# Kernel optimization log

Hardware: AMD Instinct MI355X
Metric: run time of the kernel (lower is better)

The kernel has to match this reference:

```python
import jax, jax.numpy as jnp
import numpy as np

R = 16
ALPHA = 32.0


def setup_inputs() -> dict:
    key = jax.random.key(0)
    k1, k2, k3, k4, k5 = jax.random.split(key, 5)
    in_f, out_f = 4096, 11008
    x = jax.random.normal(k1, (8192, in_f), dtype=jnp.float32)
    W = jax.random.normal(k2, (out_f, in_f), dtype=jnp.float32) * 0.02
    bias = jax.random.normal(k3, (out_f,), dtype=jnp.float32) * 0.02
    B = jax.random.normal(k4, (out_f, R), dtype=jnp.float32) * 0.01
    A = jax.random.normal(k5, (R, in_f), dtype=jnp.float32) * 0.01
    return {"x": x, "W": W, "bias": bias, "B": B, "A": A}


def reference(x, W, bias, B, A):
    # Faithful to original: materialize full-rank delta lora_mat = B @ A (out x in),
    # then h = x @ W^T + bias + (x @ lora_mat^T) * (alpha / r).
    lora_mat = jnp.matmul(B, A)                    # [out, in]
    out = jnp.matmul(x, W.T) + bias                # [tokens, out]
    lora_out = jnp.matmul(x, lora_mat.T) * (ALPHA / R)
    return out + lora_out
```

## Files before the change

### kernel.cpp

```cpp
#include <hip/hip_runtime.h>
#include <stdint.h>
#include <stddef.h>

#define M_TOK 8192
#define K_IN  4096
#define N_OUT 11008

typedef __attribute__((ext_vector_type(8))) short   short8;
typedef __attribute__((ext_vector_type(4))) float   floatx4;

#define AS1(p) ((const __attribute__((address_space(1))) void*)(p))
#define AS3(p) ((__attribute__((address_space(3))) void*)(p))

__device__ __forceinline__ unsigned short f2bf_rne(float f) {
  union { float f; unsigned u; } v; v.f = f;
  unsigned r = v.u + 0x7FFFu + ((v.u >> 16) & 1u);
  return (unsigned short)(r >> 16);
}

__device__ __forceinline__ unsigned long long pack4(float a, float b, float c, float d) {
  return (unsigned long long)f2bf_rne(a)
       | ((unsigned long long)f2bf_rne(b) << 16)
       | ((unsigned long long)f2bf_rne(c) << 32)
       | ((unsigned long long)f2bf_rne(d) << 48);
}

__global__ void cast_x_kernel(const float* __restrict__ x,
                              unsigned long long* __restrict__ xb) {
  size_t idx = (size_t)blockIdx.x * blockDim.x + threadIdx.x;
  const float4 v = ((const float4*)x)[idx];
  xb[idx] = pack4(v.x, v.y, v.z, v.w);
}

__global__ void wprime_kernel(const float* __restrict__ W,
                              const float* __restrict__ B,
                              const float* __restrict__ A,
                              unsigned long long* __restrict__ wp) {
  const int o   = blockIdx.x;
  const int col = blockIdx.y * 1024 + threadIdx.x * 4;
  float4 acc = *(const float4*)(W + (size_t)o * K_IN + col);
#pragma unroll
  for (int r = 0; r < 16; ++r) {
    const float b2 = 2.0f * B[o * 16 + r];
    const float4 a4 = *(const float4*)(A + (size_t)r * K_IN + col);
    acc.x += b2 * a4.x; acc.y += b2 * a4.y;
    acc.z += b2 * a4.z; acc.w += b2 * a4.w;
  }
  wp[((size_t)o * K_IN + col) >> 2] = pack4(acc.x, acc.y, acc.z, acc.w);
}

__global__ __launch_bounds__(256) void lora_gemm(
    const unsigned short* __restrict__ Xb,
    const unsigned short* __restrict__ Wp,
    const float* __restrict__ bias,
    float* __restrict__ out) {
  __shared__ __align__(16) unsigned short As[128 * 32];
  __shared__ __align__(16) unsigned short Bs[128 * 32];

  const int tid  = threadIdx.x;
  const int m0   = blockIdx.y * 128;
  const int n0   = blockIdx.x * 128;
  const int wid  = tid >> 6;
  const int lane = tid & 63;
  const int wm   = (wid >> 1) * 64;
  const int wn   = (wid & 1) * 64;
  const int lrow = lane & 15;
  const int quad = lane >> 4;

  floatx4 acc[4][4];
#pragma unroll
  for (int i = 0; i < 4; ++i)
#pragma unroll
    for (int j = 0; j < 4; ++j)
      acc[i][j] = (floatx4){0.f, 0.f, 0.f, 0.f};

  const int r0 = tid >> 2;
  const int s0 = (tid & 3) * 8;
  const unsigned short* pa = Xb + (size_t)(m0 + r0) * K_IN + s0;
  const unsigned short* pb = Wp + (size_t)(n0 + r0) * K_IN + s0;

  const unsigned short* pAf = As + (wm + lrow) * 32 + quad * 8;
  const unsigned short* pBf = Bs + (wn + lrow) * 32 + quad * 8;

  for (int kt = 0; kt < K_IN / 32; ++kt) {
    __builtin_amdgcn_global_load_lds(AS1(pa),                    AS3(As + tid * 8),        16, 0, 0);
    __builtin_amdgcn_global_load_lds(AS1(pa + (size_t)64 * K_IN), AS3(As + tid * 8 + 2048), 16, 0, 0);
    __builtin_amdgcn_global_load_lds(AS1(pb),                    AS3(Bs + tid * 8),        16, 0, 0);
    __builtin_amdgcn_global_load_lds(AS1(pb + (size_t)64 * K_IN), AS3(Bs + tid * 8 + 2048), 16, 0, 0);
    pa += 32; pb += 32;
    __syncthreads();

    short8 a[4], b[4];
#pragma unroll
    for (int mi = 0; mi < 4; ++mi)
      a[mi] = *(const short8*)(pAf + mi * 16 * 32);
#pragma unroll
    for (int ni = 0; ni < 4; ++ni)
      b[ni] = *(const short8*)(pBf + ni * 16 * 32);

#pragma unroll
    for (int mi = 0; mi < 4; ++mi)
#pragma unroll
      for (int ni = 0; ni < 4; ++ni)
        acc[mi][ni] = __builtin_amdgcn_mfma_f32_16x16x32_bf16(a[mi], b[ni], acc[mi][ni], 0, 0, 0);

    __syncthreads();
  }

  float bv[4];
#pragma unroll
  for (int ni = 0; ni < 4; ++ni)
    bv[ni] = bias[n0 + wn + ni * 16 + lrow];

#pragma unroll
  for (int mi = 0; mi < 4; ++mi) {
    const int rbase = m0 + wm + mi * 16 + quad * 4;
#pragma unroll
    for (int ni = 0; ni < 4; ++ni) {
      const int col = n0 + wn + ni * 16 + lrow;
#pragma unroll
      for (int r = 0; r < 4; ++r)
        out[(size_t)(rbase + r) * N_OUT + col] = acc[mi][ni][r] + bv[ni];
    }
  }
}

extern "C" void kernel_launch(void* const* d_in, const int* in_sizes, int n_in,
                              void* d_out, int out_size, void* d_ws, size_t ws_size,
                              hipStream_t stream) {
  const float* x    = (const float*)d_in[0];
  const float* W    = (const float*)d_in[1];
  const float* bias = (const float*)d_in[2];
  const float* B    = (const float*)d_in[3];
  const float* A    = (const float*)d_in[4];
  float* out = (float*)d_out;

  unsigned short* xb = (unsigned short*)d_ws;
  unsigned short* wp = (unsigned short*)((char*)d_ws + (size_t)M_TOK * K_IN * 2);

  cast_x_kernel<<<(M_TOK * K_IN / 4) / 256, 256, 0, stream>>>(
      x, (unsigned long long*)xb);
  wprime_kernel<<<dim3(N_OUT, K_IN / 1024), 256, 0, stream>>>(
      W, B, A, (unsigned long long*)wp);
  lora_gemm<<<dim3(N_OUT / 128, M_TOK / 128), 256, 0, stream>>>(
      xb, wp, bias, out);
}
```

Baseline: 1.572 ms.

## Use 256x256 tiles with triple-buffered LDS pipeline and swizzled block mapping

Rewrites the GEMM to use 512-thread workgroups computing 256x256 output tiles. Global-to-LDS loads are triple-buffered two k-steps ahead, with manual vmcnt waits and a single barrier per step. MFMA sections are raised in priority, and the block index is swizzled into groups of 8 M-tiles for L2 reuse. The aim is to hide load latency, halve barriers, and raise arithmetic intensity per byte loaded. The cost is heavier register use (32 accumulators per thread) and 96KB of LDS per block.

```diff
diff --git a/kernel.cpp b/kernel.cpp
--- a/kernel.cpp
+++ b/kernel.cpp
@@ -5,6 +5,11 @@
 #define M_TOK 8192
 #define K_IN  4096
 #define N_OUT 11008
+
+#define KT   (K_IN / 32)
+#define NTN  43
+#define NTM  32
+#define NWG  (NTN * NTM)
 
 typedef __attribute__((ext_vector_type(8))) short   short8;
 typedef __attribute__((ext_vector_type(4))) float   floatx4;
@@ -49,80 +54,120 @@
   wp[((size_t)o * K_IN + col) >> 2] = pack4(acc.x, acc.y, acc.z, acc.w);
 }
 
-__global__ __launch_bounds__(256) void lora_gemm(
+__global__ __launch_bounds__(512, 2) void lora_gemm(
     const unsigned short* __restrict__ Xb,
     const unsigned short* __restrict__ Wp,
     const float* __restrict__ bias,
     float* __restrict__ out) {
-  __shared__ __align__(16) unsigned short As[128 * 32];
-  __shared__ __align__(16) unsigned short Bs[128 * 32];
+  __shared__ __align__(16) unsigned short lds[3 * 16384];
 
   const int tid  = threadIdx.x;
-  const int m0   = blockIdx.y * 128;
-  const int n0   = blockIdx.x * 128;
+  const int lane = tid & 63;
   const int wid  = tid >> 6;
-  const int lane = tid & 63;
-  const int wm   = (wid >> 1) * 64;
-  const int wn   = (wid & 1) * 64;
   const int lrow = lane & 15;
   const int quad = lane >> 4;
+  const int wm   = wid >> 2;
+  const int wn   = wid & 3;
 
-  floatx4 acc[4][4];
+  const int bid = blockIdx.x;
+  const int sw  = (bid & 7) * (NWG / 8) + (bid >> 3);
+  const int grp = sw / (8 * NTN);
+  const int rem = sw - grp * (8 * NTN);
+  const int m0  = (grp * 8 + (rem & 7)) * 256;
+  const int n0  = (rem >> 3) * 256;
+
+  const int rowS = ((tid >> 6) << 4) | (tid & 15);
+  const int kseg = ((tid >> 4) & 3) << 3;
+  const unsigned short* pa = Xb + (size_t)(m0 + rowS) * K_IN + kseg;
+  const unsigned short* pb = Wp + (size_t)(n0 + rowS) * K_IN + kseg;
+  unsigned short* dA = lds + tid * 8;
+  unsigned short* dB = lds + 8192 + tid * 8;
+
+  const unsigned short* fA = lds + ((wm * 8) * 64 + lane) * 8;
+  const unsigned short* fB = lds + 8192 + ((wn * 4) * 64 + lane) * 8;
+
+#define STAGE_A(q, t) do {                                                                  \
+    const unsigned short* s_ = pa + (size_t)(t) * 32;                                       \
+    __builtin_amdgcn_global_load_lds(AS1(s_),                        AS3(dA + (q) * 16384),        16, 0, 0); \
+    __builtin_amdgcn_global_load_lds(AS1(s_ + (size_t)128 * K_IN),   AS3(dA + (q) * 16384 + 4096), 16, 0, 0); \
+  } while (0)
+#define STAGE_B(q, t) do {                                                                  \
+    const unsigned short* s_ = pb + (size_t)(t) * 32;                                       \
+    __builtin_amdgcn_global_load_lds(AS1(s_),                        AS3(dB + (q) * 16384),        16, 0, 0); \
+    __builtin_amdgcn_global_load_lds(AS1(s_ + (size_t)128 * K_IN),   AS3(dB + (q) * 16384 + 4096), 16, 0, 0); \
+  } while (0)
+
+  floatx4 acc[8][4];
 #pragma unroll
-  for (int i = 0; i < 4; ++i)
+  for (int i = 0; i < 8; ++i)
 #pragma unroll
     for (int j = 0; j < 4; ++j)
       acc[i][j] = (floatx4){0.f, 0.f, 0.f, 0.f};
 
-  const int r0 = tid >> 2;
-  const int s0 = (tid & 3) * 8;
-  const unsigned short* pa = Xb + (size_t)(m0 + r0) * K_IN + s0;
-  const unsigned short* pb = Wp + (size_t)(n0 + r0) * K_IN + s0;
+  STAGE_A(0, 0); STAGE_B(0, 0);
+  STAGE_A(1, 1); STAGE_B(1, 1);
+  asm volatile("s_waitcnt vmcnt(4)" ::: "memory");
+  __builtin_amdgcn_s_barrier();
+  asm volatile("" ::: "memory");
 
-  const unsigned short* pAf = As + (wm + lrow) * 32 + quad * 8;
-  const unsigned short* pBf = Bs + (wn + lrow) * 32 + quad * 8;
+  int cur = 0, nxt = 2;
+  for (int t = 0; t < KT; ++t) {
+    const unsigned short* fAc = fA + cur * 16384;
+    const unsigned short* fBc = fB + cur * 16384;
 
-  for (int kt = 0; kt < K_IN / 32; ++kt) {
-    __builtin_amdgcn_global_load_lds(AS1(pa),                    AS3(As + tid * 8),        16, 0, 0);
-    __builtin_amdgcn_global_load_lds(AS1(pa + (size_t)64 * K_IN), AS3(As + tid * 8 + 2048), 16, 0, 0);
-    __builtin_amdgcn_global_load_lds(AS1(pb),                    AS3(Bs + tid * 8),        16, 0, 0);
-    __builtin_amdgcn_global_load_lds(AS1(pb + (size_t)64 * K_IN), AS3(Bs + tid * 8 + 2048), 16, 0, 0);
-    pa += 32; pb += 32;
-    __syncthreads();
-
-    short8 a[4], b[4];
+    if (t + 2 < KT) STAGE_A(nxt, t + 2);
+    short8 b[4], a[4];
 #pragma unroll
-    for (int mi = 0; mi < 4; ++mi)
-      a[mi] = *(const short8*)(pAf + mi * 16 * 32);
+    for (int ni = 0; ni < 4; ++ni) b[ni] = *(const short8*)(fBc + ni * 512);
 #pragma unroll
-    for (int ni = 0; ni < 4; ++ni)
-      b[ni] = *(const short8*)(pBf + ni * 16 * 32);
-
+    for (int mi = 0; mi < 4; ++mi) a[mi] = *(const short8*)(fAc + mi * 512);
+    __builtin_amdgcn_s_setprio(1);
 #pragma unroll
     for (int mi = 0; mi < 4; ++mi)
 #pragma unroll
       for (int ni = 0; ni < 4; ++ni)
         acc[mi][ni] = __builtin_amdgcn_mfma_f32_16x16x32_bf16(a[mi], b[ni], acc[mi][ni], 0, 0, 0);
+    __builtin_amdgcn_s_setprio(0);
 
-    __syncthreads();
+    if (t + 2 < KT) STAGE_B(nxt, t + 2);
+    short8 a2[4];
+#pragma unroll
+    for (int mi = 0; mi < 4; ++mi) a2[mi] = *(const short8*)(fAc + (4 + mi) * 512);
+    __builtin_amdgcn_s_setprio(1);
+#pragma unroll
+    for (int mi = 0; mi < 4; ++mi)
+#pragma unroll
+      for (int ni = 0; ni < 4; ++ni)
+        acc[4 + mi][ni] = __builtin_amdgcn_mfma_f32_16x16x32_bf16(a2[mi], b[ni], acc[4 + mi][ni], 0, 0, 0);
+    __builtin_amdgcn_s_setprio(0);
+
+    if (t < KT - 2) { asm volatile("s_waitcnt vmcnt(4)" ::: "memory"); }
+    else           { asm volatile("s_waitcnt vmcnt(0)" ::: "memory"); }
+    __builtin_amdgcn_s_barrier();
+    asm volatile("" ::: "memory");
+
+    cur = (cur == 2) ? 0 : cur + 1;
+    nxt = (nxt == 2) ? 0 : nxt + 1;
   }
 
   float bv[4];
 #pragma unroll
   for (int ni = 0; ni < 4; ++ni)
-    bv[ni] = bias[n0 + wn + ni * 16 + lrow];
+    bv[ni] = bias[n0 + wn * 64 + ni * 16 + lrow];
 
 #pragma unroll
-  for (int mi = 0; mi < 4; ++mi) {
-    const int rbase = m0 + wm + mi * 16 + quad * 4;
+  for (int mi = 0; mi < 8; ++mi) {
+    const int rbase = m0 + wm * 128 + mi * 16 + quad * 4;
 #pragma unroll
     for (int ni = 0; ni < 4; ++ni) {
-      const int col = n0 + wn + ni * 16 + lrow;
+      const int col = n0 + wn * 64 + ni * 16 + lrow;
 #pragma unroll
       for (int r = 0; r < 4; ++r)
         out[(size_t)(rbase + r) * N_OUT + col] = acc[mi][ni][r] + bv[ni];
     }
   }
+#undef STAGE_A
+#undef STAGE_B
 }
 
 extern "C" void kernel_launch(void* const* d_in, const int* in_sizes, int n_in,
@@ -142,6 +187,5 @@
       x, (unsigned long long*)xb);
   wprime_kernel<<<dim3(N_OUT, K_IN / 1024), 256, 0, stream>>>(
       W, B, A, (unsigned long long*)wp);
-  lora_gemm<<<dim3(N_OUT / 128, M_TOK / 128), 256, 0, stream>>>(
-      xb, wp, bias, out);
+  lora_gemm<<<dim3(NWG), 512, 0, stream>>>(xb, wp, bias, out);
 }
```

Result: faster. 1.428 ms (-9.2%).
